# Kernel tuning notes

Measured on AMD Instinct MI355X. Metric: run time of the kernel, lower is better.

The kernel has to match this reference:

```python
import jax, jax.numpy as jnp
import numpy as np

N = 100000   # nodes
E = 1600000  # edges (avg degree 16)
D_IN, D_HID, D_OUT = 128, 128, 64
BN_EPS = 1e-5


def setup_inputs() -> dict:
    key = jax.random.key(0)
    ks = jax.random.split(key, 12)
    nf_mat = jax.random.normal(ks[0], (N, D_IN), dtype=jnp.float32)
    edge_index = jax.random.randint(ks[1], (2, E), 0, N, dtype=jnp.int32)
    # pre-normalized adjacency weights (GCNConv normalize=True is folded into conv_mat here)
    edge_weight = jax.random.uniform(ks[2], (E,), dtype=jnp.float32) * (1.0 / 16.0)
    def glorot(k, fan_in, fan_out):
        s = jnp.sqrt(6.0 / (fan_in + fan_out)).astype(jnp.float32)
        return jax.random.uniform(k, (fan_in, fan_out), dtype=jnp.float32, minval=-s, maxval=s)
    return {
        "nf_mat": nf_mat,
        "edge_index": edge_index,
        "edge_weight": edge_weight,
        "W0": glorot(ks[3], D_IN, D_HID), "b0": jnp.zeros((D_HID,), jnp.float32),
        "W1": glorot(ks[4], D_HID, D_HID), "b1": jnp.zeros((D_HID,), jnp.float32),
        "W2": glorot(ks[5], D_HID, D_OUT), "b2": jnp.zeros((D_OUT,), jnp.float32),
        "gamma0": jnp.ones((D_HID,), jnp.float32), "beta0": jnp.zeros((D_HID,), jnp.float32),
        "gamma1": jnp.ones((D_HID,), jnp.float32), "beta1": jnp.zeros((D_HID,), jnp.float32),
    }


def _gcn_conv(x, W, b, src, dst, w):
    # GCNConv: aggregate A_norm @ (x W) + b over the sparse edge list
    h = x @ W                                   # [N, F_out]
    msg = h[src] * w[:, None]                   # [E, F_out] gather + scale
    agg = jax.ops.segment_sum(msg, dst, num_segments=N)  # scatter-add -> [N, F_out]
    return agg + b


def _batchnorm(x, gamma, beta):
    # BatchNorm1d over node dimension (training-mode batch statistics, biased var)
    mu = jnp.mean(x, axis=0)
    var = jnp.mean(jnp.square(x - mu), axis=0)
    return gamma * (x - mu) * jax.lax.rsqrt(var + BN_EPS) + beta


def reference(nf_mat, edge_index, edge_weight, W0, b0, W1, b1, W2, b2,
              gamma0, beta0, gamma1, beta1):
    src, dst = edge_index[0], edge_index[1]
    x = nf_mat
    # layer 0: conv -> BN -> ReLU (dropout is identity in eval)
    x = _gcn_conv(x, W0, b0, src, dst, edge_weight)
    x = jax.nn.relu(_batchnorm(x, gamma0, beta0))
    # layer 1
    x = _gcn_conv(x, W1, b1, src, dst, edge_weight)
    x = jax.nn.relu(_batchnorm(x, gamma1, beta1))
    # final conv, then cross-node sum
    x = _gcn_conv(x, W2, b2, src, dst, edge_weight)
    return jnp.sum(x, axis=0)  # [D_OUT]
```

## Files before the change

### kernel.cpp

```cpp
#include <hip/hip_runtime.h>

#define BN_EPS 1e-5f

#define NPB 512
#define NPB_SHIFT 9
#define PB 512
#define MAXB 256
#define NSLICE 16

typedef __attribute__((ext_vector_type(8))) short short8;
typedef __attribute__((ext_vector_type(4))) float floatx4;
typedef __attribute__((ext_vector_type(2))) float floatx2;

__device__ __forceinline__ unsigned short f2bf(float f) {
    unsigned u = __float_as_uint(f);
    unsigned r = u + 0x7FFFu + ((u >> 16) & 1u);
    return (unsigned short)(r >> 16);
}
__device__ __forceinline__ float blo(unsigned v) { return __uint_as_float(v << 16); }
__device__ __forceinline__ float bhi(unsigned v) { return __uint_as_float(v & 0xffff0000u); }

__device__ __forceinline__ uint2 pk8_fp8(const float4 v0, const float4 v1) {
    int lo = 0, hi = 0;
    lo = __builtin_amdgcn_cvt_pk_fp8_f32(v0.x, v0.y, lo, false);
    lo = __builtin_amdgcn_cvt_pk_fp8_f32(v0.z, v0.w, lo, true);
    hi = __builtin_amdgcn_cvt_pk_fp8_f32(v1.x, v1.y, hi, false);
    hi = __builtin_amdgcn_cvt_pk_fp8_f32(v1.z, v1.w, hi, true);
    return make_uint2((unsigned)lo, (unsigned)hi);
}

__global__ __launch_bounds__(256) void wconv(
    const float* __restrict__ W0, const float* __restrict__ W1,
    unsigned short* __restrict__ wt0, unsigned short* __restrict__ wt1,
    float* __restrict__ stats)
{
    const int idx = blockIdx.x * 256 + threadIdx.x;
    const int n = idx >> 7, k = idx & 127;
    wt0[idx] = f2bf(W0[k * 128 + n]);
    wt1[idx] = f2bf(W1[k * 128 + n]);
    if (blockIdx.x < 10) {
        const int o = (blockIdx.x * 256 + threadIdx.x) * 4;
        *(float4*)&stats[o] = make_float4(0.f, 0.f, 0.f, 0.f);
    }
}

__global__ __launch_bounds__(256) void gemm0(
    const float* __restrict__ A, const unsigned short* __restrict__ Wt,
    uint2* __restrict__ C, int M)
{
    __shared__ char lds[53248];
    unsigned short* Al = (unsigned short*)lds;
    unsigned short* Wl = (unsigned short*)(lds + 17408);
    float* Cl = (float*)lds;

    const int tid = threadIdx.x;
    const int r0 = blockIdx.x * 64;

#pragma unroll
    for (int i = 0; i < 16; ++i) {
        const int idx = i * 256 + tid;
        const int n = idx >> 5, q = idx & 31;
        const ushort4 v = ((const ushort4*)Wt)[idx];
        *(ushort4*)&Wl[n * 136 + q * 4] = v;
    }
#pragma unroll
    for (int i = 0; i < 8; ++i) {
        const int row = i * 8 + (tid >> 5), q = tid & 31;
        const int gr = r0 + row;
        float4 v = (gr < M) ? ((const float4*)A)[(size_t)gr * 32 + q]
                            : make_float4(0.f, 0.f, 0.f, 0.f);
        ushort4 o;
        o.x = f2bf(v.x); o.y = f2bf(v.y); o.z = f2bf(v.z); o.w = f2bf(v.w);
        *(ushort4*)&Al[row * 136 + q * 4] = o;
    }
    __syncthreads();

    const int wave = tid >> 6, lane = tid & 63;
    const int lrow = lane & 15, quad = lane >> 4;
    const int n0 = wave * 32;

    floatx4 acc[4][2];
#pragma unroll
    for (int mt = 0; mt < 4; ++mt)
#pragma unroll
        for (int t = 0; t < 2; ++t)
#pragma unroll
            for (int j = 0; j < 4; ++j) acc[mt][t][j] = 0.f;

#pragma unroll
    for (int c = 0; c < 4; ++c) {
        const int k0 = c * 32;
        const short8 b0 = *(const short8*)&Wl[(n0 + lrow) * 136 + k0 + quad * 8];
        const short8 b1 = *(const short8*)&Wl[(n0 + 16 + lrow) * 136 + k0 + quad * 8];
#pragma unroll
        for (int mt = 0; mt < 4; ++mt) {
            const short8 a = *(const short8*)&Al[(mt * 16 + lrow) * 136 + k0 + quad * 8];
            acc[mt][0] = __builtin_amdgcn_mfma_f32_16x16x32_bf16(a, b0, acc[mt][0], 0, 0, 0);
            acc[mt][1] = __builtin_amdgcn_mfma_f32_16x16x32_bf16(a, b1, acc[mt][1], 0, 0, 0);
        }
    }
    __syncthreads();

#pragma unroll
    for (int mt = 0; mt < 4; ++mt)
#pragma unroll
        for (int t = 0; t < 2; ++t)
#pragma unroll
            for (int j = 0; j < 4; ++j)
                Cl[(mt * 16 + quad * 4 + j) * 132 + n0 + t * 16 + lrow] = acc[mt][t][j];
    __syncthreads();

#pragma unroll
    for (int i = 0; i < 4; ++i) {
        const int row = i * 16 + (tid >> 4);
        const int c0 = (tid & 15) * 8;
        const int gr = r0 + row;
        if (gr < M) {
            const float4 v0 = *(float4*)&Cl[row * 132 + c0];
            const float4 v1 = *(float4*)&Cl[row * 132 + c0 + 4];
            C[(size_t)gr * 16 + (c0 >> 3)] = pk8_fp8(v0, v1);
        }
    }
}

__global__ __launch_bounds__(256) void gemm1(
    const unsigned* __restrict__ Ab, const unsigned short* __restrict__ Wt,
    uint2* __restrict__ C,
    const float* __restrict__ sum, const float* __restrict__ sq,
    const float* __restrict__ g, const float* __restrict__ be,
    int M, int N)
{
    __shared__ char lds[53248];
    unsigned short* Al = (unsigned short*)lds;
    unsigned short* Wl = (unsigned short*)(lds + 17408);
    float* AscL = (float*)(lds + 52224);
    float* AshL = AscL + 128;
    float* Cl = (float*)lds;

    const int tid = threadIdx.x;
    const int r0 = blockIdx.x * 64;

    if (tid < 128) {
        float s = 0.f, q = 0.f;
#pragma unroll
        for (int k = 0; k < NSLICE; ++k) {
            s += sum[k * 128 + tid];
            q += sq[k * 128 + tid];
        }
        const float invN = 1.0f / (float)N;
        const float m = s * invN;
        const float var = q * invN - m * m;
        const float rs = rsqrtf(var + BN_EPS);
        AscL[tid] = g[tid] * rs;
        AshL[tid] = be[tid] - g[tid] * m * rs;
    }
    __syncthreads();

#pragma unroll
    for (int i = 0; i < 16; ++i) {
        const int idx = i * 256 + tid;
        const int n = idx >> 5, q = idx & 31;
        const ushort4 v = ((const ushort4*)Wt)[idx];
        *(ushort4*)&Wl[n * 136 + q * 4] = v;
    }
#pragma unroll
    for (int i = 0; i < 4; ++i) {
        const int idx = i * 256 + tid;
        const int row = idx >> 4, qc = idx & 15;
        const int gr = r0 + row;
        uint4 v = (gr < M) ? ((const uint4*)Ab)[(size_t)gr * 16 + qc]
                           : make_uint4(0, 0, 0, 0);
        const float4 a0 = *(const float4*)&AscL[qc * 8];
        const float4 a1 = *(const float4*)&AscL[qc * 8 + 4];
        const float4 b0 = *(const float4*)&AshL[qc * 8];
        const float4 b1 = *(const float4*)&AshL[qc * 8 + 4];
        float x0 = fmaxf(fmaf(a0.x, blo(v.x), b0.x), 0.f);
        float x1 = fmaxf(fmaf(a0.y, bhi(v.x), b0.y), 0.f);
        float x2 = fmaxf(fmaf(a0.z, blo(v.y), b0.z), 0.f);
        float x3 = fmaxf(fmaf(a0.w, bhi(v.y), b0.w), 0.f);
        float x4 = fmaxf(fmaf(a1.x, blo(v.z), b1.x), 0.f);
        float x5 = fmaxf(fmaf(a1.y, bhi(v.z), b1.y), 0.f);
        float x6 = fmaxf(fmaf(a1.z, blo(v.w), b1.z), 0.f);
        float x7 = fmaxf(fmaf(a1.w, bhi(v.w), b1.w), 0.f);
        uint4 o;
        o.x = (unsigned)f2bf(x0) | ((unsigned)f2bf(x1) << 16);
        o.y = (unsigned)f2bf(x2) | ((unsigned)f2bf(x3) << 16);
        o.z = (unsigned)f2bf(x4) | ((unsigned)f2bf(x5) << 16);
        o.w = (unsigned)f2bf(x6) | ((unsigned)f2bf(x7) << 16);
        *(uint4*)&Al[row * 136 + qc * 8] = o;
    }
    __syncthreads();

    const int wave = tid >> 6, lane = tid & 63;
    const int lrow = lane & 15, quad = lane >> 4;
    const int n0 = wave * 32;

    floatx4 acc[4][2];
#pragma unroll
    for (int mt = 0; mt < 4; ++mt)
#pragma unroll
        for (int t = 0; t < 2; ++t)
#pragma unroll
            for (int j = 0; j < 4; ++j) acc[mt][t][j] = 0.f;

#pragma unroll
    for (int c = 0; c < 4; ++c) {
        const int k0 = c * 32;
        const short8 b0 = *(const short8*)&Wl[(n0 + lrow) * 136 + k0 + quad * 8];
        const short8 b1 = *(const short8*)&Wl[(n0 + 16 + lrow) * 136 + k0 + quad * 8];
#pragma unroll
        for (int mt = 0; mt < 4; ++mt) {
            const short8 a = *(const short8*)&Al[(mt * 16 + lrow) * 136 + k0 + quad * 8];
            acc[mt][0] = __builtin_amdgcn_mfma_f32_16x16x32_bf16(a, b0, acc[mt][0], 0, 0, 0);
            acc[mt][1] = __builtin_amdgcn_mfma_f32_16x16x32_bf16(a, b1, acc[mt][1], 0, 0, 0);
        }
    }
    __syncthreads();

#pragma unroll
    for (int mt = 0; mt < 4; ++mt)
#pragma unroll
        for (int t = 0; t < 2; ++t)
#pragma unroll
            for (int j = 0; j < 4; ++j)
                Cl[(mt * 16 + quad * 4 + j) * 132 + n0 + t * 16 + lrow] = acc[mt][t][j];
    __syncthreads();

#pragma unroll
    for (int i = 0; i < 4; ++i) {
        const int row = i * 16 + (tid >> 4);
        const int c0 = (tid & 15) * 8;
        const int gr = r0 + row;
        if (gr < M) {
            const float4 v0 = *(float4*)&Cl[row * 132 + c0];
            const float4 v1 = *(float4*)&Cl[row * 132 + c0 + 4];
            C[(size_t)gr * 16 + (c0 >> 3)] = pk8_fp8(v0, v1);
        }
    }
}


__global__ __launch_bounds__(512) void bucket_hist(
    const int* __restrict__ src, const int* __restrict__ dst,
    int* __restrict__ cntD, int* __restrict__ cntS, int E, int B, int chunk)
{
    __shared__ int hD[MAXB], hS[MAXB];
    const int tid = threadIdx.x;
    for (int i = tid; i < B; i += 512) { hD[i] = 0; hS[i] = 0; }
    __syncthreads();
    const int lo = blockIdx.x * chunk;
    const int hi = min(E, lo + chunk);
    for (int e = lo + tid; e < hi; e += 512) {
        atomicAdd(&hD[dst[e] >> NPB_SHIFT], 1);
        atomicAdd(&hS[src[e] >> NPB_SHIFT], 1);
    }
    __syncthreads();
    for (int i = tid; i < B; i += 512) {
        cntD[i * PB + blockIdx.x] = hD[i];
        cntS[i * PB + blockIdx.x] = hS[i];
    }
}

__global__ __launch_bounds__(256) void bucket_base(
    const int* __restrict__ cntD, const int* __restrict__ cntS,
    int* __restrict__ baseD, int* __restrict__ baseS, int B, int E)
{
    __shared__ int lD[256], lS[256];
    const int tid = threadIdx.x;
    int sD = 0, sS = 0;
    if (tid < B) {
        const int4* pD = (const int4*)(cntD + tid * PB);
        const int4* pS = (const int4*)(cntS + tid * PB);
        for (int j = 0; j < PB / 4; ++j) {
            const int4 a = pD[j], b = pS[j];
            sD += a.x + a.y + a.z + a.w;
            sS += b.x + b.y + b.z + b.w;
        }
    }
    lD[tid] = sD; lS[tid] = sS;
    __syncthreads();
    for (int st = 1; st < 256; st <<= 1) {
        const int vD = (tid >= st) ? lD[tid - st] : 0;
        const int vS = (tid >= st) ? lS[tid - st] : 0;
        __syncthreads();
        lD[tid] += vD; lS[tid] += vS;
        __syncthreads();
    }
    if (tid < B) { baseD[tid] = lD[tid] - sD; baseS[tid] = lS[tid] - sS; }
    if (tid == 0) { baseD[B] = E; baseS[B] = E; }
}

__global__ __launch_bounds__(256) void bucket_cursor(
    int* __restrict__ cntD, int* __restrict__ cntS,
    const int* __restrict__ baseD, const int* __restrict__ baseS, int B)
{
    int b = blockIdx.x;
    int* cnt; const int* base;
    if (b < B) { cnt = cntD; base = baseD; }
    else       { cnt = cntS; base = baseS; b -= B; }
    __shared__ int ls[256];
    const int tid = threadIdx.x;
    const int c0 = cnt[b * PB + 2 * tid];
    const int c1 = cnt[b * PB + 2 * tid + 1];
    const int s = c0 + c1;
    ls[tid] = s;
    __syncthreads();
    for (int st = 1; st < 256; st <<= 1) {
        const int v = (tid >= st) ? ls[tid - st] : 0;
        __syncthreads();
        ls[tid] += v;
        __syncthreads();
    }
    const int excl = ls[tid] - s + base[b];
    cnt[b * PB + 2 * tid] = excl;
    cnt[b * PB + 2 * tid + 1] = excl + c0;
}

__global__ __launch_bounds__(512) void bucket_place(
    const int* __restrict__ src, const int* __restrict__ dst,
    const float* __restrict__ ew,
    const int* __restrict__ curD, const int* __restrict__ curS,
    uint2* __restrict__ bktD, uint2* __restrict__ bktS, int E, int B, int chunk)
{
    __shared__ int cD[MAXB], cS[MAXB];
    const int tid = threadIdx.x;
    for (int i = tid; i < B; i += 512) {
        cD[i] = curD[i * PB + blockIdx.x];
        cS[i] = curS[i * PB + blockIdx.x];
    }
    __syncthreads();
    const int lo = blockIdx.x * chunk;
    const int hi = min(E, lo + chunk);
    for (int e = lo + tid; e < hi; e += 512) {
        const int s = src[e], d = dst[e];
        const unsigned wb = __float_as_uint(ew[e]);
        const int pd = atomicAdd(&cD[d >> NPB_SHIFT], 1);
        bktD[pd] = make_uint2(((unsigned)s << NPB_SHIFT) | (unsigned)(d & (NPB - 1)), wb);
        const int ps = atomicAdd(&cS[s >> NPB_SHIFT], 1);
        bktS[ps] = make_uint2((unsigned)(s & (NPB - 1)), wb);
    }
}

__global__ __launch_bounds__(256) void bucket_sortcw(
    const uint2* __restrict__ bktD, const int* __restrict__ baseD,
    int* __restrict__ rp, int2* __restrict__ packed,
    const uint2* __restrict__ bktS, const int* __restrict__ baseS,
    float* __restrict__ cw, int N, int B)
{
    const int tid = threadIdx.x;
    if (blockIdx.x >= B) {
        const int b = blockIdx.x - B;
        const int lo = baseS[b], hi = baseS[b + 1];
        __shared__ float sm[NPB];
        sm[2 * tid] = 0.f; sm[2 * tid + 1] = 0.f;
        __syncthreads();
        for (int i = lo + tid; i < hi; i += 256) {
            const uint2 r = bktS[i];
            atomicAdd(&sm[r.x], __uint_as_float(r.y));
        }
        __syncthreads();
        const int n0 = b * NPB + 2 * tid;
        if (n0 < N)     cw[n0]     = sm[2 * tid];
        if (n0 + 1 < N) cw[n0 + 1] = sm[2 * tid + 1];
        return;
    }
    const int b = blockIdx.x;
    const int lo = baseD[b], hi = baseD[b + 1];
    __shared__ int cnt[NPB], cur[NPB];
    __shared__ int ls[256];
    cnt[2 * tid] = 0; cnt[2 * tid + 1] = 0;
    __syncthreads();
    for (int i = lo + tid; i < hi; i += 256)
        atomicAdd(&cnt[bktD[i].x & (NPB - 1)], 1);
    __syncthreads();
    const int c0 = cnt[2 * tid], c1 = cnt[2 * tid + 1];
    const int s = c0 + c1;
    ls[tid] = s;
    __syncthreads();
    for (int st = 1; st < 256; st <<= 1) {
        const int v = (tid >= st) ? ls[tid - st] : 0;
        __syncthreads();
        ls[tid] += v;
        __syncthreads();
    }
    const int excl = ls[tid] - s;
    const int n0 = b * NPB + 2 * tid;
    if (n0 < N)     rp[n0]     = lo + excl + c0;
    if (n0 + 1 < N) rp[n0 + 1] = lo + excl + c0 + c1;
    cur[2 * tid]     = lo + excl;
    cur[2 * tid + 1] = lo + excl + c0;
    __syncthreads();
    for (int i = lo + tid; i < hi; i += 256) {
        const uint2 r = bktD[i];
        const int pos = atomicAdd(&cur[r.x & (NPB - 1)], 1);
        packed[pos] = make_int2((int)(r.x >> NPB_SHIFT) << 4, (int)r.y);
    }
}


#define ACC_EDGE(V, W, A) do { \
    floatx2 w2_; w2_.x = (W); w2_.y = (W); \
    floatx2 f_; \
    f_ = __builtin_amdgcn_cvt_pk_f32_fp8((int)(V).x, false); \
    A[0] = f_ * w2_ + A[0]; \
    f_ = __builtin_amdgcn_cvt_pk_f32_fp8((int)(V).x, true);  \
    A[1] = f_ * w2_ + A[1]; \
    f_ = __builtin_amdgcn_cvt_pk_f32_fp8((int)(V).y, false); \
    A[2] = f_ * w2_ + A[2]; \
    f_ = __builtin_amdgcn_cvt_pk_f32_fp8((int)(V).y, true);  \
    A[3] = f_ * w2_ + A[3]; \
} while (0)

__global__ __launch_bounds__(256) void aggq(
    const int2* __restrict__ packed, const int* __restrict__ rp,
    const uint2* __restrict__ h2, uint4* __restrict__ aggb4,
    float* __restrict__ sum, float* __restrict__ sq, int N)
{
    __shared__ int2 eb[16][65];
    __shared__ float lsum[512], lsq[512];

    const int tid = threadIdx.x;
    const int lane = tid & 63, wave = tid >> 6;
    const int sub = lane >> 4;
    const int u = lane & 15;
    const int wq = wave * 4 + sub;
    const int nb0 = blockIdx.x * 32;
    const int nX = nb0 + wq * 2, nY = nX + 1;
    int2* ebq = eb[wq];

    int rpv = 0;
    {
        const int idx = nb0 - 1 + lane;
        if (lane <= 32 && idx >= 0 && idx < N) rpv = rp[idx];
    }
    const int sX = __shfl(rpv, 2 * wq, 64);
    const int eX = __shfl(rpv, 2 * wq + 1, 64);
    const int eYr = __shfl(rpv, 2 * wq + 2, 64);
    const int sY = eX;
    const int dXf = max(eX - sX, 0), dYf = max(eYr - sY, 0);
    const int eXe = sX + dXf, eYe = sY + dYf;

    {
        int2 r;
        r = (u      < dXf) ? packed[sX + u]      : make_int2(0, 0); ebq[u]      = r;
        r = (u + 16 < dXf) ? packed[sX + 16 + u] : make_int2(0, 0); ebq[16 + u] = r;
        r = (u      < dYf) ? packed[sY + u]      : make_int2(0, 0); ebq[32 + u] = r;
        r = (u + 16 < dYf) ? packed[sY + 16 + u] : make_int2(0, 0); ebq[48 + u] = r;
    }

    floatx2 aX[4], aY[4];
#pragma unroll
    for (int k = 0; k < 4; ++k) { aX[k] = 0.f; aY[k] = 0.f; }

    const int cX = min(dXf, 32), cY = min(dYf, 32);
    const int jmax = (cX > cY) ? cX : cY;

    for (int j = 0; j < jmax; j += 4) {
        const int2 x0 = ebq[j],      x1 = ebq[j + 1];
        const int2 x2 = ebq[j + 2],  x3 = ebq[j + 3];
        const int2 y0 = ebq[32 + j],     y1 = ebq[32 + j + 1];
        const int2 y2 = ebq[32 + j + 2], y3 = ebq[32 + j + 3];
        const uint2 vx0 = h2[(size_t)(unsigned)(x0.x + u)];
        const uint2 vx1 = h2[(size_t)(unsigned)(x1.x + u)];
        const uint2 vx2 = h2[(size_t)(unsigned)(x2.x + u)];
        const uint2 vx3 = h2[(size_t)(unsigned)(x3.x + u)];
        const uint2 vy0 = h2[(size_t)(unsigned)(y0.x + u)];
        const uint2 vy1 = h2[(size_t)(unsigned)(y1.x + u)];
        const uint2 vy2 = h2[(size_t)(unsigned)(y2.x + u)];
        const uint2 vy3 = h2[(size_t)(unsigned)(y3.x + u)];
        ACC_EDGE(vx0, __int_as_float(x0.y), aX);
        ACC_EDGE(vx1, __int_as_float(x1.y), aX);
        ACC_EDGE(vx2, __int_as_float(x2.y), aX);
        ACC_EDGE(vx3, __int_as_float(x3.y), aX);
        ACC_EDGE(vy0, __int_as_float(y0.y), aY);
        ACC_EDGE(vy1, __int_as_float(y1.y), aY);
        ACC_EDGE(vy2, __int_as_float(y2.y), aY);
        ACC_EDGE(vy3, __int_as_float(y3.y), aY);
    }

    for (int base = sX + 32; base < eXe; base += 32) {
        const int rem = eXe - base;
        int2 r;
        r = (u      < rem) ? packed[base + u]      : make_int2(0, 0); ebq[u]      = r;
        r = (u + 16 < rem) ? packed[base + 16 + u] : make_int2(0, 0); ebq[16 + u] = r;
        const int cc = min(rem, 32);
        for (int j = 0; j < cc; j += 4) {
            const int2 x0 = ebq[j], x1 = ebq[j + 1], x2 = ebq[j + 2], x3 = ebq[j + 3];
            const uint2 v0 = h2[(size_t)(unsigned)(x0.x + u)];
            const uint2 v1 = h2[(size_t)(unsigned)(x1.x + u)];
            const uint2 v2 = h2[(size_t)(unsigned)(x2.x + u)];
            const uint2 v3 = h2[(size_t)(unsigned)(x3.x + u)];
            ACC_EDGE(v0, __int_as_float(x0.y), aX);
            ACC_EDGE(v1, __int_as_float(x1.y), aX);
            ACC_EDGE(v2, __int_as_float(x2.y), aX);
            ACC_EDGE(v3, __int_as_float(x3.y), aX);
        }
    }
    for (int base = sY + 32; base < eYe; base += 32) {
        const int rem = eYe - base;
        int2 r;
        r = (u      < rem) ? packed[base + u]      : make_int2(0, 0); ebq[32 + u] = r;
        r = (u + 16 < rem) ? packed[base + 16 + u] : make_int2(0, 0); ebq[48 + u] = r;
        const int cc = min(rem, 32);
        for (int j = 0; j < cc; j += 4) {
            const int2 y0 = ebq[32 + j], y1 = ebq[32 + j + 1];
            const int2 y2 = ebq[32 + j + 2], y3 = ebq[32 + j + 3];
            const uint2 v0 = h2[(size_t)(unsigned)(y0.x + u)];
            const uint2 v1 = h2[(size_t)(unsigned)(y1.x + u)];
            const uint2 v2 = h2[(size_t)(unsigned)(y2.x + u)];
            const uint2 v3 = h2[(size_t)(unsigned)(y3.x + u)];
            ACC_EDGE(v0, __int_as_float(y0.y), aY);
            ACC_EDGE(v1, __int_as_float(y1.y), aY);
            ACC_EDGE(v2, __int_as_float(y2.y), aY);
            ACC_EDGE(v3, __int_as_float(y3.y), aY);
        }
    }

    if (nX < N) {
        uint4 o;
        o.x = (unsigned)f2bf(aX[0].x) | ((unsigned)f2bf(aX[0].y) << 16);
        o.y = (unsigned)f2bf(aX[1].x) | ((unsigned)f2bf(aX[1].y) << 16);
        o.z = (unsigned)f2bf(aX[2].x) | ((unsigned)f2bf(aX[2].y) << 16);
        o.w = (unsigned)f2bf(aX[3].x) | ((unsigned)f2bf(aX[3].y) << 16);
        aggb4[(size_t)nX * 16 + u] = o;
    }
    if (nY < N) {
        uint4 o;
        o.x = (unsigned)f2bf(aY[0].x) | ((unsigned)f2bf(aY[0].y) << 16);
        o.y = (unsigned)f2bf(aY[1].x) | ((unsigned)f2bf(aY[1].y) << 16);
        o.z = (unsigned)f2bf(aY[2].x) | ((unsigned)f2bf(aY[2].y) << 16);
        o.w = (unsigned)f2bf(aY[3].x) | ((unsigned)f2bf(aY[3].y) << 16);
        aggb4[(size_t)nY * 16 + u] = o;
    }

    floatx2 cs0 = aX[0] + aY[0], cs1 = aX[1] + aY[1];
    floatx2 cs2 = aX[2] + aY[2], cs3 = aX[3] + aY[3];
    floatx2 cq0 = aX[0] * aX[0] + aY[0] * aY[0];
    floatx2 cq1 = aX[1] * aX[1] + aY[1] * aY[1];
    floatx2 cq2 = aX[2] * aX[2] + aY[2] * aY[2];
    floatx2 cq3 = aX[3] * aX[3] + aY[3] * aY[3];
#define XRED(V) \
    V.x += __shfl_xor(V.x, 16, 64); V.y += __shfl_xor(V.y, 16, 64); \
    V.x += __shfl_xor(V.x, 32, 64); V.y += __shfl_xor(V.y, 32, 64);
    XRED(cs0) XRED(cs1) XRED(cs2) XRED(cs3)
    XRED(cq0) XRED(cq1) XRED(cq2) XRED(cq3)
#undef XRED
    const floatx2 ws = (sub == 0) ? cs0 : (sub == 1) ? cs1 : (sub == 2) ? cs2 : cs3;
    const floatx2 wwq = (sub == 0) ? cq0 : (sub == 1) ? cq1 : (sub == 2) ? cq2 : cq3;
    const int col = u * 8 + 2 * sub;
    lsum[wave * 128 + col] = ws.x;  lsum[wave * 128 + col + 1] = ws.y;
    lsq[wave * 128 + col]  = wwq.x; lsq[wave * 128 + col + 1]  = wwq.y;
    __syncthreads();
    if (tid < 128) {
        float s = 0.f, q = 0.f;
#pragma unroll
        for (int i = 0; i < 4; ++i) {
            s += lsum[i * 128 + tid];
            q += lsq[i * 128 + tid];
        }
        const int sl = (blockIdx.x & (NSLICE - 1)) * 128;
        atomicAdd(&sum[sl + tid], s);
        atomicAdd(&sq[sl + tid], q);
    }
}

__global__ __launch_bounds__(256) void wcolsum_bf16(
    const uint2* __restrict__ xb2, const float* __restrict__ cw,
    const float* __restrict__ sum1, const float* __restrict__ sq1,
    const float* __restrict__ g, const float* __restrict__ be,
    float* __restrict__ sout, int N)
{
    __shared__ float Aaf[128], Baf[128];
    __shared__ float4 ls[256];
    const int tid = threadIdx.x;
    if (tid < 128) {
        float s = 0.f, q = 0.f;
#pragma unroll
        for (int k = 0; k < NSLICE; ++k) {
            s += sum1[k * 128 + tid];
            q += sq1[k * 128 + tid];
        }
        const float invN = 1.0f / (float)N;
        const float m = s * invN;
        const float var = q * invN - m * m;
        const float rs = rsqrtf(var + BN_EPS);
        Aaf[tid] = g[tid] * rs;
        Baf[tid] = be[tid] - g[tid] * m * rs;
    }
    __syncthreads();
    const int u2 = tid & 31;
    const int half = (tid >> 5) & 1;
    const int rr = tid >> 6;
    const float4 A = *(const float4*)&Aaf[u2 * 4];
    const float4 Bv = *(const float4*)&Baf[u2 * 4];
    float4 s = make_float4(0.f, 0.f, 0.f, 0.f);
    for (int row = blockIdx.x * 8 + rr * 2 + half; row < N; row += gridDim.x * 8) {
        const uint2 v = xb2[(size_t)row * 32 + u2];
        const float c = cw[row];
        s.x = fmaf(c, fmaxf(fmaf(A.x, blo(v.x), Bv.x), 0.f), s.x);
        s.y = fmaf(c, fmaxf(fmaf(A.y, bhi(v.x), Bv.y), 0.f), s.y);
        s.z = fmaf(c, fmaxf(fmaf(A.z, blo(v.y), Bv.z), 0.f), s.z);
        s.w = fmaf(c, fmaxf(fmaf(A.w, bhi(v.y), Bv.w), 0.f), s.w);
    }
    ls[tid] = s;
    __syncthreads();
    if (tid < 32) {
        float4 a = ls[tid];
#pragma unroll
        for (int k = 1; k < 8; ++k) {
            const float4 b = ls[tid + 32 * k];
            a.x += b.x; a.y += b.y; a.z += b.z; a.w += b.w;
        }
        float* so = sout + (blockIdx.x & (NSLICE - 1)) * 128 + tid * 4;
        atomicAdd(&so[0], a.x);
        atomicAdd(&so[1], a.y);
        atomicAdd(&so[2], a.z);
        atomicAdd(&so[3], a.w);
    }
}

__global__ void final_out(
    const float* __restrict__ s, const float* __restrict__ W2,
    const float* __restrict__ b2, float* __restrict__ out, int N, int Dout)
{
    __shared__ float sv[128];
    const int j = threadIdx.x;
    {
        float a = 0.f;
#pragma unroll
        for (int k = 0; k < NSLICE; ++k) a += s[k * 128 + j];
        sv[j] = a;
    }
    __syncthreads();
    if (j < Dout) {
        float acc = 0.f;
        for (int f = 0; f < 128; ++f) acc = fmaf(sv[f], W2[f * Dout + j], acc);
        out[j] = acc + (float)N * b2[j];
    }
}

extern "C" void kernel_launch(void* const* d_in, const int* in_sizes, int n_in,
                              void* d_out, int out_size, void* d_ws, size_t ws_size,
                              hipStream_t stream)
{
    const float* nf  = (const float*)d_in[0];
    const int*   ei  = (const int*)d_in[1];
    const float* ew  = (const float*)d_in[2];
    const float* W0  = (const float*)d_in[3];
    const float* W1  = (const float*)d_in[5];
    const float* W2  = (const float*)d_in[7];
    const float* b2  = (const float*)d_in[8];
    const float* g0  = (const float*)d_in[9];
    const float* be0 = (const float*)d_in[10];
    const float* g1  = (const float*)d_in[11];
    const float* be1 = (const float*)d_in[12];

    const int N = in_sizes[0] / 128;
    const int E = in_sizes[2];
    const int* srcI = ei;
    const int* dstI = ei + E;

    const int B = (N + NPB - 1) / NPB;
    const int chunk = (E + PB - 1) / PB;

    const size_t HB = ((size_t)N * 128 * 2 + 255) & ~(size_t)255;
    const size_t NA = ((size_t)N * sizeof(int) + 255) & ~(size_t)255;
    const size_t CB = (((size_t)B * PB * 4) + 255) & ~(size_t)255;
    char* ws = (char*)d_ws;
    size_t off = 0;
    float* cw    = (float*)(ws + off); off += NA;
    int*   rp    = (int*)  (ws + off); off += NA;
    float* stats = (float*)(ws + off); off += 40960;
    int*   cntD  = (int*)  (ws + off); off += CB;
    int*   cntS  = (int*)  (ws + off); off += CB;
    int*   baseD = (int*)  (ws + off); off += 2048;
    int*   baseS = (int*)  (ws + off); off += 2048;
    uint2* hbuf  = (uint2*)(ws + off); off += HB;
    unsigned* aggb = (unsigned*)(ws + off); off += HB;
    int2*  packed = (int2*)(ws + off); off += (size_t)E * 8;
    uint2* bktD  = (uint2*)(ws + off); off += (size_t)E * 8;
    uint2* bktS  = (uint2*)(ws + off); off += (size_t)E * 8;
    unsigned short* wt0 = (unsigned short*)(ws + off); off += 32768;
    unsigned short* wt1 = (unsigned short*)(ws + off); off += 32768;
    (void)ws_size;

    float* sum0 = stats + 0 * NSLICE * 128;
    float* sq0  = stats + 1 * NSLICE * 128;
    float* sum1 = stats + 2 * NSLICE * 128;
    float* sq1  = stats + 3 * NSLICE * 128;
    float* svec = stats + 4 * NSLICE * 128;

    const int gemmGrid = (N + 63) / 64;
    const int aggGrid  = (N + 31) / 32;

    bucket_hist<<<PB, 512, 0, stream>>>(srcI, dstI, cntD, cntS, E, B, chunk);
    bucket_base<<<1, 256, 0, stream>>>(cntD, cntS, baseD, baseS, B, E);
    bucket_cursor<<<2 * B, 256, 0, stream>>>(cntD, cntS, baseD, baseS, B);
    bucket_place<<<PB, 512, 0, stream>>>(srcI, dstI, ew, cntD, cntS, bktD, bktS, E, B, chunk);
    bucket_sortcw<<<2 * B, 256, 0, stream>>>(bktD, baseD, rp, packed,
                                             bktS, baseS, cw, N, B);
    wconv<<<64, 256, 0, stream>>>(W0, W1, wt0, wt1, stats);

    gemm0<<<gemmGrid, 256, 0, stream>>>(nf, wt0, hbuf, N);
    aggq<<<aggGrid, 256, 0, stream>>>(
        packed, rp, (const uint2*)hbuf, (uint4*)aggb, sum0, sq0, N);

    gemm1<<<gemmGrid, 256, 0, stream>>>(aggb, wt1, hbuf, sum0, sq0, g0, be0, N, N);
    aggq<<<aggGrid, 256, 0, stream>>>(
        packed, rp, (const uint2*)hbuf, (uint4*)aggb, sum1, sq1, N);

    wcolsum_bf16<<<2048, 256, 0, stream>>>((const uint2*)aggb, cw, sum1, sq1,
                                           g1, be1, svec, N);
    final_out<<<1, 128, 0, stream>>>(svec, W2, b2, (float*)d_out, N, out_size);
}
```

Measured before the change: 342.4 us.

## Write-combine bucket scatter in LDS before flushing to global buckets

The bucket_place kernel no longer scatters each edge record straight to its global bucket slot. It now stages records in per-bucket shared-memory buffers of 16 entries. After each 512-edge tile, one thread per bucket flushes whole groups of 8 records contiguously to global memory, and records that overflow the buffer go straight to global. The aim is to turn scattered 8-byte stores into contiguous runs that fill memory sectors better. In exchange it adds two block barriers per tile and serial per-thread flush loops, and it needs the bucket count to stay at or below 200.

Measured after the change: 335.7 us. About the same (-2.0%).

```diff
diff --git a/kernel.cpp b/kernel.cpp
--- a/kernel.cpp
+++ b/kernel.cpp
@@ -6,6 +6,8 @@
 #define NPB_SHIFT 9
 #define PB 512
 #define MAXB 256
+#define WCB 200
+#define WCCAP 16
 #define NSLICE 16
 
 typedef __attribute__((ext_vector_type(8))) short short8;
@@ -322,22 +324,63 @@
     const int* __restrict__ curD, const int* __restrict__ curS,
     uint2* __restrict__ bktD, uint2* __restrict__ bktS, int E, int B, int chunk)
 {
-    __shared__ int cD[MAXB], cS[MAXB];
+    __shared__ uint2 bufD[WCB][WCCAP + 1], bufS[WCB][WCCAP + 1];
+    __shared__ int tailD[WCB], tailS[WCB], gcurD[WCB], gcurS[WCB];
     const int tid = threadIdx.x;
     for (int i = tid; i < B; i += 512) {
-        cD[i] = curD[i * PB + blockIdx.x];
-        cS[i] = curS[i * PB + blockIdx.x];
+        gcurD[i] = curD[i * PB + blockIdx.x];
+        gcurS[i] = curS[i * PB + blockIdx.x];
+        tailD[i] = 0; tailS[i] = 0;
     }
     __syncthreads();
     const int lo = blockIdx.x * chunk;
     const int hi = min(E, lo + chunk);
-    for (int e = lo + tid; e < hi; e += 512) {
-        const int s = src[e], d = dst[e];
-        const unsigned wb = __float_as_uint(ew[e]);
-        const int pd = atomicAdd(&cD[d >> NPB_SHIFT], 1);
-        bktD[pd] = make_uint2(((unsigned)s << NPB_SHIFT) | (unsigned)(d & (NPB - 1)), wb);
-        const int ps = atomicAdd(&cS[s >> NPB_SHIFT], 1);
-        bktS[ps] = make_uint2((unsigned)(s & (NPB - 1)), wb);
+    const int nt = (hi - lo + 511) >> 9;
+    for (int t = 0; t < nt; ++t) {
+        const int e = lo + t * 512 + tid;
+        if (e < hi) {
+            const int s = src[e], d = dst[e];
+            const unsigned wb = __float_as_uint(ew[e]);
+            const int bd = d >> NPB_SHIFT;
+            const uint2 rd = make_uint2(((unsigned)s << NPB_SHIFT) | (unsigned)(d & (NPB - 1)), wb);
+            const int pd = atomicAdd(&tailD[bd], 1);
+            if (pd < WCCAP) bufD[bd][pd] = rd;
+            else            bktD[gcurD[bd] + pd] = rd;
+            const int bs = s >> NPB_SHIFT;
+            const uint2 rs = make_uint2((unsigned)(s & (NPB - 1)), wb);
+            const int ps = atomicAdd(&tailS[bs], 1);
+            if (ps < WCCAP) bufS[bs][ps] = rs;
+            else            bktS[gcurS[bs] + ps] = rs;
+        }
+        __syncthreads();
+        const bool last = (t == nt - 1);
+        if (tid < B) {
+            {
+                const int tl = tailD[tid];
+                const int nb = min(tl, WCCAP);
+                const int k = last ? nb : (nb & ~7);
+                const int base = gcurD[tid];
+                for (int i = 0; i < k; ++i) bktD[base + i] = bufD[tid][i];
+                const int adv = (tl > WCCAP) ? tl : k;
+                const int left = (tl > WCCAP) ? 0 : (tl - k);
+                for (int i = 0; i < left; ++i) bufD[tid][i] = bufD[tid][k + i];
+                gcurD[tid] = base + adv;
+                tailD[tid] = left;
+            }
+            {
+                const int tl = tailS[tid];
+                const int nb = min(tl, WCCAP);
+                const int k = last ? nb : (nb & ~7);
+                const int base = gcurS[tid];
+                for (int i = 0; i < k; ++i) bktS[base + i] = bufS[tid][i];
+                const int adv = (tl > WCCAP) ? tl : k;
+                const int left = (tl > WCCAP) ? 0 : (tl - k);
+                for (int i = 0; i < left; ++i) bufS[tid][i] = bufS[tid][k + i];
+                gcurS[tid] = base + adv;
+                tailS[tid] = left;
+            }
+        }
+        __syncthreads();
     }
 }
 
```
